# Performance work log

Hardware: AMD Instinct MI355X
Metric: run time of the kernel (lower is better)

## Reference

```python
import jax, jax.numpy as jnp
import numpy as np

DIM = 192
HEADS = 6
EPS = 1e-12  # torch F.normalize eps


def setup_inputs() -> dict:
    key = jax.random.key(0)
    k1, k2, k3, k4 = jax.random.split(key, 4)
    x = jax.random.normal(k1, (8, DIM, 128, 128), dtype=jnp.float32)
    # qkv: Conv2d(dim, 3*dim, k=3, pad=1, bias=False) -> OIHW weight
    qkv_w = jax.random.normal(k2, (3 * DIM, DIM, 3, 3), dtype=jnp.float32) * (1.0 / np.sqrt(DIM * 9))
    # project_out: Conv2d(dim, dim, k=1, bias=True)
    proj_w = jax.random.normal(k3, (DIM, DIM, 1, 1), dtype=jnp.float32) * (1.0 / np.sqrt(DIM))
    proj_b = jax.random.normal(k4, (DIM,), dtype=jnp.float32) * 0.01
    temperature = jnp.ones((HEADS, 1, 1), dtype=jnp.float32)
    return {"x": x, "qkv_w": qkv_w, "proj_w": proj_w, "proj_b": proj_b, "temperature": temperature}


def _conv2d(x, w, padding):
    return jax.lax.conv_general_dilated(
        x, w, window_strides=(1, 1), padding=padding,
        dimension_numbers=("NCHW", "OIHW", "NCHW"))


def reference(x, qkv_w, proj_w, proj_b, temperature):
    n, c, h, w = x.shape
    ch = c // HEADS  # channels per head
    qkv = _conv2d(x, qkv_w, ((1, 1), (1, 1)))  # [n, 3c, h, w]
    q, k, v = jnp.split(qkv, 3, axis=1)
    # n (head c) h w -> n head c (h*w)
    def to_heads(t):
        return t.reshape(n, HEADS, ch, h * w)
    q, k, v = to_heads(q), to_heads(k), to_heads(v)
    # L2 normalize over HW (last dim)
    q = q / jnp.maximum(jnp.linalg.norm(q, axis=-1, keepdims=True), EPS)
    k = k / jnp.maximum(jnp.linalg.norm(k, axis=-1, keepdims=True), EPS)
    # channel-wise cosine attention: [n, head, c, c]
    attn = jnp.einsum("nhcp,nhdp->nhcd", q, k) * temperature
    attn = jax.nn.softmax(attn, axis=-1)
    out = jnp.einsum("nhcd,nhdp->nhcp", attn, v)  # [n, head, ch, hw]
    out = out.reshape(n, c, h, w)
    out = _conv2d(out, proj_w, ((0, 0), (0, 0))) + proj_b[None, :, None, None]
    return out
```

## Files before the change

### kernel.cpp

```cpp
#include <hip/hip_runtime.h>
#include <stdint.h>

#define DIM 192
#define HEADS 6
#define HW 16384
#define CO 576
#define K9 1728
#define CQK 384

typedef __attribute__((ext_vector_type(8))) short bf16x8;
typedef __attribute__((ext_vector_type(4))) float f32x4;

__device__ __forceinline__ unsigned short f2bf(float f) {
  union { float f; unsigned u; } v; v.f = f;
  unsigned r = v.u + 0x7FFFu + ((v.u >> 16) & 1u);
  return (unsigned short)(r >> 16);
}

__device__ __forceinline__ void gll16(const void* g, void* l) {
  __builtin_amdgcn_global_load_lds(
      (const __attribute__((address_space(1))) unsigned int*)g,
      (__attribute__((address_space(3))) unsigned int*)l, 16, 0, 0);
}

__global__ __launch_bounds__(256) void k_reorder_w(const float* __restrict__ w,
                                                   unsigned short* __restrict__ wbf) {
  int g = blockIdx.x * 256 + threadIdx.x;
  if (g >= CO * K9) return;
  int o = g / K9, rem = g % K9;
  int rs = rem / DIM, ci = rem % DIM;
  wbf[g] = f2bf(w[(o * DIM + ci) * 9 + rs]);
}

__global__ __launch_bounds__(256) void k_nhwc(const float* __restrict__ x,
                                              unsigned short* __restrict__ xbf) {
  int g = blockIdx.x * 256 + threadIdx.x;
  int xcol = g & 127;
  int t2 = g >> 7;
  int c24 = t2 % 24;
  int t3 = t2 / 24;
  int y = t3 & 127;
  int n = t3 >> 7;
  union { unsigned short u[8]; uint4 v; } pk;
#pragma unroll
  for (int i = 0; i < 8; ++i)
    pk.u[i] = f2bf(x[((size_t)(n * DIM + c24 * 8 + i) * 128 + y) * 128 + xcol]);
  *(uint4*)&xbf[(size_t)((n * 128 + y) * 128 + xcol) * DIM + c24 * 8] = pk.v;
}

__global__ __launch_bounds__(256, 4) void k_conv(const unsigned short* __restrict__ xbf,
                                                 const unsigned short* __restrict__ wbf,
                                                 const char* __restrict__ zeros,
                                                 unsigned short* __restrict__ qkv,
                                                 unsigned short* __restrict__ vt) {
  __shared__ char smem[40960];
  const int tid = threadIdx.x;
  const int lane = tid & 63;
  const int wv = tid >> 6;
  const int lane15 = lane & 15;
  const int lgrp = lane >> 4;

  int p = blockIdx.x;
  int xcd = p & 7;
  int slot = p >> 3;
  int work = xcd * 576 + slot;
  int cblk = work % 9;
  int g = work / 9;
  const int by = g & 63;
  const int n = g >> 6;
  const int c0 = cblk * 64;
  const int y0 = by * 2;

  f32x4 acc[4][4] = {};

  auto stage = [&](int t) {
    int rs = t / 3;
    int ci0 = (t % 3) * 64;
    int r = rs / 3, s = rs % 3;
#pragma unroll
    for (int rr = 0; rr < 2; ++rr) {
      int off = tid * 16 + rr * 4096;
      int row = off >> 7;
      int scb = (off & 127) ^ ((row & 7) << 4);
      const char* gp = (const char*)wbf + (size_t)((c0 + row) * K9 + rs * DIM + ci0) * 2 + scb;
      gll16(gp, smem + rr * 4096 + wv * 1024);
    }
    int yb = y0 + r - 1;
#pragma unroll
    for (int rr = 0; rr < 8; ++rr) {
      int off = tid * 16 + rr * 4096;
      int prow = off >> 7;
      int scb = (off & 127) ^ ((prow & 7) << 4);
      int yy = yb + (prow >> 7);
      int xx = (prow & 127) + s - 1;
      const char* gp;
      if (yy < 0 || yy > 127 || xx < 0 || xx > 127)
        gp = zeros + scb;
      else
        gp = (const char*)xbf + (size_t)(((n * 128 + yy) * 128 + xx) * DIM + ci0) * 2 + scb;
      gll16(gp, smem + 8192 + rr * 4096 + wv * 1024);
    }
  };

  auto compute = [&]() {
    char* Ab = smem;
    char* Bb = smem + 8192;
#pragma unroll
    for (int k32 = 0; k32 < 2; ++k32) {
      int kb = k32 * 64 + lgrp * 16;
      bf16x8 a[4], b[4];
#pragma unroll
      for (int m = 0; m < 4; ++m) {
        int row = m * 16 + lane15;
        a[m] = *(bf16x8*)(Ab + row * 128 + (kb ^ ((row & 7) << 4)));
      }
#pragma unroll
      for (int nb = 0; nb < 4; ++nb) {
        int pp = wv * 64 + nb * 16 + lane15;
        b[nb] = *(bf16x8*)(Bb + pp * 128 + (kb ^ ((pp & 7) << 4)));
      }
#pragma unroll
      for (int m = 0; m < 4; ++m)
#pragma unroll
        for (int nb = 0; nb < 4; ++nb)
          acc[m][nb] = __builtin_amdgcn_mfma_f32_16x16x32_bf16(a[m], b[nb], acc[m][nb], 0, 0, 0);
    }
  };

  for (int t = 0; t < 27; ++t) {
    stage(t);
    __syncthreads();
    compute();
    __syncthreads();
  }

  char* st = smem;
  if (cblk < 6) {
#pragma unroll
    for (int m = 0; m < 4; ++m)
#pragma unroll
      for (int nb = 0; nb < 4; ++nb) {
        int pix = wv * 64 + nb * 16 + lane15;
#pragma unroll
        for (int j = 0; j < 4; ++j) {
          int c = m * 16 + lgrp * 4 + j;
          *(unsigned short*)(st + c * 512 + ((pix * 2) ^ ((c & 7) << 4))) = f2bf(acc[m][nb][j]);
        }
      }
    __syncthreads();
    int c = tid >> 2, q4 = tid & 3;
    char* dst = (char*)qkv + ((size_t)(n * CQK + c0 + c) * HW + by * 256 + q4 * 64) * 2;
#pragma unroll
    for (int i = 0; i < 8; ++i) {
      uint4 vv = *(uint4*)(st + c * 512 + ((q4 * 128 + i * 16) ^ ((c & 7) << 4)));
      *(uint4*)(dst + i * 16) = vv;
    }
  } else {
    int dg0 = c0 - 384;
#pragma unroll
    for (int m = 0; m < 4; ++m)
#pragma unroll
      for (int nb = 0; nb < 4; ++nb) {
        int pix = wv * 64 + nb * 16 + lane15;
        int cl = m * 16 + lgrp * 4;
        union { unsigned short u[4]; uint2 v; } pk;
#pragma unroll
        for (int j = 0; j < 4; ++j) pk.u[j] = f2bf(acc[m][nb][j]);
        *(uint2*)(st + pix * 128 + ((cl * 2) ^ ((pix & 7) << 4))) = pk.v;
      }
    __syncthreads();
    char* dst = (char*)vt + ((size_t)(n * HW + by * 256 + tid) * DIM + dg0) * 2;
#pragma unroll
    for (int i = 0; i < 8; ++i) {
      uint4 vv = *(uint4*)(st + tid * 128 + ((i * 16) ^ ((tid & 7) << 4)));
      *(uint4*)(dst + i * 16) = vv;
    }
  }
}

__global__ __launch_bounds__(256) void k_gram(const unsigned short* __restrict__ qkv,
                                              float* __restrict__ G) {
  const int pc = blockIdx.x, h = blockIdx.y, n = blockIdx.z;
  const int tid = threadIdx.x, lane = tid & 63, wv = tid >> 6;
  const int lane15 = lane & 15, lgrp = lane >> 4;
  const unsigned short* base[4];
#pragma unroll
  for (int mi = 0; mi < 4; ++mi) {
    int ch = mi * 16 + lane15;
    int cg = (ch < 32) ? (h * 32 + ch) : (DIM + h * 32 + ch - 32);
    base[mi] = qkv + (size_t)(n * CQK + cg) * HW;
  }
  f32x4 acc[4][4] = {};
  int pbase = pc * 2048 + wv * 512;
  for (int st = 0; st < 16; ++st) {
    int p = pbase + st * 32 + lgrp * 8;
    bf16x8 f[4];
#pragma unroll
    for (int mi = 0; mi < 4; ++mi) f[mi] = *(const bf16x8*)(base[mi] + p);
#pragma unroll
    for (int mi = 0; mi < 4; ++mi)
#pragma unroll
      for (int ni = 0; ni < 4; ++ni)
        acc[mi][ni] = __builtin_amdgcn_mfma_f32_16x16x32_bf16(f[mi], f[ni], acc[mi][ni], 0, 0, 0);
  }
  float* Gm = G + (size_t)(n * HEADS + h) * 4096;
#pragma unroll
  for (int mi = 0; mi < 4; ++mi)
#pragma unroll
    for (int ni = 0; ni < 4; ++ni)
#pragma unroll
      for (int j = 0; j < 4; ++j) {
        int row = mi * 16 + lgrp * 4 + j;
        int col = ni * 16 + lane15;
        atomicAdd(&Gm[row * 64 + col], acc[mi][ni][j]);
      }
}

__global__ __launch_bounds__(256) void k_attnm(const float* __restrict__ G,
                                               const float* __restrict__ temp,
                                               const float* __restrict__ projw,
                                               unsigned short* __restrict__ Mbf) {
  __shared__ float attn_s[HEADS][32][32];
  int n = blockIdx.x, tid = threadIdx.x;
  if (tid < 192) {
    int h = tid >> 5, c = tid & 31;
    const float* Gm = G + (size_t)(n * HEADS + h) * 4096;
    float nq = fmaxf(sqrtf(Gm[c * 64 + c]), 1e-12f);
    float tp = temp[h];
    float l[32];
    float mx = -1e30f;
#pragma unroll
    for (int d = 0; d < 32; ++d) {
      float nk = fmaxf(sqrtf(Gm[(32 + d) * 64 + 32 + d]), 1e-12f);
      l[d] = Gm[c * 64 + 32 + d] / (nq * nk) * tp;
      mx = fmaxf(mx, l[d]);
    }
    float sum = 0.f;
#pragma unroll
    for (int d = 0; d < 32; ++d) { l[d] = expf(l[d] - mx); sum += l[d]; }
    float inv = 1.f / sum;
#pragma unroll
    for (int d = 0; d < 32; ++d) attn_s[h][c][d] = l[d] * inv;
  }
  __syncthreads();
  for (int idx = tid; idx < DIM * DIM; idx += 256) {
    int o = idx / DIM, dg = idx % DIM;
    int h = dg >> 5, d = dg & 31;
    float s = 0.f;
#pragma unroll
    for (int c = 0; c < 32; ++c)
      s += projw[o * DIM + h * 32 + c] * attn_s[h][c][d];
    Mbf[(size_t)(n * DIM + o) * DIM + dg] = f2bf(s);
  }
}

__global__ __launch_bounds__(256, 4) void k_out(const unsigned short* __restrict__ Mbf,
                                                const unsigned short* __restrict__ vt,
                                                const float* __restrict__ bias,
                                                float* __restrict__ out) {
  __shared__ char smem[40960];
  const int tid = threadIdx.x;
  const int lane = tid & 63;
  const int wv = tid >> 6;
  const int lane15 = lane & 15;
  const int lgrp = lane >> 4;
  const int c0 = blockIdx.x * 64;
  const int p0 = blockIdx.y * 256;
  const int n = blockIdx.z;

  f32x4 acc[4][4] = {};

  auto stage = [&](int t) {
#pragma unroll
    for (int rr = 0; rr < 2; ++rr) {
      int off = tid * 16 + rr * 4096;
      int row = off >> 7;
      int scb = (off & 127) ^ ((row & 7) << 4);
      const char* gp = (const char*)Mbf + (size_t)(n * DIM + c0 + row) * 384 + t * 128 + scb;
      gll16(gp, smem + rr * 4096 + wv * 1024);
    }
#pragma unroll
    for (int rr = 0; rr < 8; ++rr) {
      int off = tid * 16 + rr * 4096;
      int prow = off >> 7;
      int scb = (off & 127) ^ ((prow & 7) << 4);
      const char* gp = (const char*)vt + (size_t)(n * HW + p0 + prow) * 384 + t * 128 + scb;
      gll16(gp, smem + 8192 + rr * 4096 + wv * 1024);
    }
  };

  auto compute = [&]() {
    char* Ab = smem;
    char* Bb = smem + 8192;
#pragma unroll
    for (int k32 = 0; k32 < 2; ++k32) {
      int kb = k32 * 64 + lgrp * 16;
      bf16x8 a[4], b[4];
#pragma unroll
      for (int m = 0; m < 4; ++m) {
        int row = m * 16 + lane15;
        a[m] = *(bf16x8*)(Ab + row * 128 + (kb ^ ((row & 7) << 4)));
      }
#pragma unroll
      for (int nb = 0; nb < 4; ++nb) {
        int pp = wv * 64 + nb * 16 + lane15;
        b[nb] = *(bf16x8*)(Bb + pp * 128 + (kb ^ ((pp & 7) << 4)));
      }
#pragma unroll
      for (int m = 0; m < 4; ++m)
#pragma unroll
        for (int nb = 0; nb < 4; ++nb)
          acc[m][nb] = __builtin_amdgcn_mfma_f32_16x16x32_bf16(a[m], b[nb], acc[m][nb], 0, 0, 0);
    }
  };

  for (int t = 0; t < 3; ++t) {
    stage(t);
    __syncthreads();
    compute();
    __syncthreads();
  }

#pragma unroll
  for (int m = 0; m < 4; ++m)
#pragma unroll
    for (int nb = 0; nb < 4; ++nb)
#pragma unroll
      for (int j = 0; j < 4; ++j) {
        int c = c0 + m * 16 + lgrp * 4 + j;
        int pix = wv * 64 + nb * 16 + lane15;
        out[(size_t)(n * DIM + c) * HW + p0 + pix] = acc[m][nb][j] + bias[c];
      }
}

extern "C" void kernel_launch(void* const* d_in, const int* in_sizes, int n_in,
                              void* d_out, int out_size, void* d_ws, size_t ws_size,
                              hipStream_t stream) {
  const float* x      = (const float*)d_in[0];
  const float* qkv_w  = (const float*)d_in[1];
  const float* proj_w = (const float*)d_in[2];
  const float* proj_b = (const float*)d_in[3];
  const float* temp   = (const float*)d_in[4];
  float* out = (float*)d_out;

  char* ws = (char*)d_ws;
  float* G            = (float*)ws;
  const char* zeros   = ws + 786432;
  unsigned short* wbf = (unsigned short*)(ws + 786688);
  unsigned short* qkv = (unsigned short*)(ws + 2777344);
  unsigned short* Mbf = (unsigned short*)(ws + 103440640);
  unsigned short* xbf = (unsigned short*)(ws + 104030464);
  unsigned short* vt  = (unsigned short*)(ws + 154362112);

  (void)hipMemsetAsync(ws, 0, 786688, stream);
  k_reorder_w<<<(CO * K9 + 255) / 256, 256, 0, stream>>>(qkv_w, wbf);
  k_nhwc<<<12288, 256, 0, stream>>>(x, xbf);
  k_conv<<<4608, 256, 0, stream>>>(xbf, wbf, zeros, qkv, vt);
  k_gram<<<dim3(8, HEADS, 8), 256, 0, stream>>>(qkv, G);
  k_attnm<<<8, 256, 0, stream>>>(G, temp, proj_w, Mbf);
  k_out<<<dim3(3, 64, 8), 256, 0, stream>>>(Mbf, vt, proj_b, out);
}
```

Before: 644.6 us.

## Stage 4-row input halo once per channel chunk and read weights directly

The conv kernel now loads a 4-row halo of input pixels (32 channels per chunk) into LDS once per channel chunk and reuses it for all nine 3x3 taps, instead of restaging a shifted input tile for each tap. Weight fragments are read straight from global memory into registers rather than through LDS. This cuts redundant global-to-LDS traffic and the barriers per tap, down from 54 to 12 per block. In exchange it adds uncoalesced global weight loads inside the MFMA loop and lowers the occupancy hint from 4 to 3.

```diff
diff --git a/kernel.cpp b/kernel.cpp
--- a/kernel.cpp
+++ b/kernel.cpp
@@ -48,12 +48,12 @@
   *(uint4*)&xbf[(size_t)((n * 128 + y) * 128 + xcol) * DIM + c24 * 8] = pk.v;
 }
 
-__global__ __launch_bounds__(256, 4) void k_conv(const unsigned short* __restrict__ xbf,
+__global__ __launch_bounds__(256, 3) void k_conv(const unsigned short* __restrict__ xbf,
                                                  const unsigned short* __restrict__ wbf,
                                                  const char* __restrict__ zeros,
                                                  unsigned short* __restrict__ qkv,
                                                  unsigned short* __restrict__ vt) {
-  __shared__ char smem[40960];
+  __shared__ char halo[4 * 8320];
   const int tid = threadIdx.x;
   const int lane = tid & 63;
   const int wv = tid >> 6;
@@ -62,8 +62,8 @@
 
   int p = blockIdx.x;
   int xcd = p & 7;
-  int slot = p >> 3;
-  int work = xcd * 576 + slot;
+  int slot0 = p >> 3;
+  int work = xcd * 576 + slot0;
   int cblk = work % 9;
   int g = work / 9;
   const int by = g & 63;
@@ -73,51 +73,48 @@
 
   f32x4 acc[4][4] = {};
 
-  auto stage = [&](int t) {
-    int rs = t / 3;
-    int ci0 = (t % 3) * 64;
-    int r = rs / 3, s = rs % 3;
-#pragma unroll
-    for (int rr = 0; rr < 2; ++rr) {
-      int off = tid * 16 + rr * 4096;
-      int row = off >> 7;
-      int scb = (off & 127) ^ ((row & 7) << 4);
-      const char* gp = (const char*)wbf + (size_t)((c0 + row) * K9 + rs * DIM + ci0) * 2 + scb;
-      gll16(gp, smem + rr * 4096 + wv * 1024);
-    }
-    int yb = y0 + r - 1;
-#pragma unroll
-    for (int rr = 0; rr < 8; ++rr) {
-      int off = tid * 16 + rr * 4096;
-      int prow = off >> 7;
-      int scb = (off & 127) ^ ((prow & 7) << 4);
-      int yy = yb + (prow >> 7);
-      int xx = (prow & 127) + s - 1;
-      const char* gp;
-      if (yy < 0 || yy > 127 || xx < 0 || xx > 127)
-        gp = zeros + scb;
-      else
-        gp = (const char*)xbf + (size_t)(((n * 128 + yy) * 128 + xx) * DIM + ci0) * 2 + scb;
-      gll16(gp, smem + 8192 + rr * 4096 + wv * 1024);
-    }
-  };
-
-  auto compute = [&]() {
-    char* Ab = smem;
-    char* Bb = smem + 8192;
-#pragma unroll
-    for (int k32 = 0; k32 < 2; ++k32) {
-      int kb = k32 * 64 + lgrp * 16;
+  if (tid < 32) {
+    int hr = tid >> 3, rem = tid & 7;
+    int side = rem >> 2, q = rem & 3;
+    *(uint4*)(halo + hr * 8320 + side * 8256 + q * 16) = make_uint4(0u, 0u, 0u, 0u);
+  }
+
+  for (int ci = 0; ci < 6; ++ci) {
+    __syncthreads();
+#pragma unroll
+    for (int hr = 0; hr < 4; ++hr) {
+      int yy = y0 - 1 + hr;
+      bool oob = (yy < 0) || (yy > 127);
+      const char* rowbase = (const char*)xbf + ((size_t)(n * 128 + yy) * 128) * 384 + ci * 64;
+#pragma unroll
+      for (int pass = 0; pass < 2; ++pass) {
+        int o = pass * 4096 + tid * 16;
+        int xx = o >> 6;
+        int slt = (o >> 4) & 3;
+        int kc = slt ^ (((xx + 1) >> 2) & 3);
+        const char* src = oob ? (const char*)zeros : rowbase + xx * 384 + kc * 16;
+        gll16(src, halo + hr * 8320 + 64 + pass * 4096 + wv * 1024);
+      }
+    }
+    __syncthreads();
+
+#pragma unroll
+    for (int rs = 0; rs < 9; ++rs) {
+      const int r = rs / 3, s = rs % 3;
       bf16x8 a[4], b[4];
 #pragma unroll
       for (int m = 0; m < 4; ++m) {
         int row = m * 16 + lane15;
-        a[m] = *(bf16x8*)(Ab + row * 128 + (kb ^ ((row & 7) << 4)));
+        a[m] = *(const bf16x8*)((const char*)wbf +
+                 (size_t)(c0 + row) * 3456 + rs * 384 + ci * 64 + lgrp * 16);
       }
 #pragma unroll
       for (int nb = 0; nb < 4; ++nb) {
-        int pp = wv * 64 + nb * 16 + lane15;
-        b[nb] = *(bf16x8*)(Bb + pp * 128 + (kb ^ ((pp & 7) << 4)));
+        int pix = wv * 64 + nb * 16 + lane15;
+        int prow = pix >> 7;
+        int cp = (pix & 127) + s;
+        b[nb] = *(const bf16x8*)(halo + (prow + r) * 8320 + cp * 64 +
+                                 ((lgrp ^ ((cp >> 2) & 3)) << 4));
       }
 #pragma unroll
       for (int m = 0; m < 4; ++m)
@@ -125,16 +122,10 @@
         for (int nb = 0; nb < 4; ++nb)
           acc[m][nb] = __builtin_amdgcn_mfma_f32_16x16x32_bf16(a[m], b[nb], acc[m][nb], 0, 0, 0);
     }
-  };
-
-  for (int t = 0; t < 27; ++t) {
-    stage(t);
-    __syncthreads();
-    compute();
-    __syncthreads();
-  }
-
-  char* st = smem;
+  }
+  __syncthreads();
+
+  char* st = halo;
   if (cblk < 6) {
 #pragma unroll
     for (int m = 0; m < 4; ++m)
```

After: 847.6 us. 31.5% more time.
